# Performance work log

Measured on AMD Instinct MI355X. Metric: run time of the kernel, lower is better.

The kernel has to match this reference:

```python
import jax, jax.numpy as jnp
import numpy as np

TEMPERATURE = 0.1
EPS = 1e-12  # matches torch F.normalize eps


def _l2_normalize(x, axis=-1):
    n = jnp.sqrt(jnp.sum(x * x, axis=axis, keepdims=True))
    return x / jnp.maximum(n, EPS)


def setup_inputs() -> dict:
    key = jax.random.key(0)
    k1, k2, k3 = jax.random.split(key, 3)
    B, K, D, M = 128, 256, 256, 4
    local_vectors = jax.random.normal(k1, (B, K, D), dtype=jnp.float32)
    prototypes = jax.random.normal(k2, (K * M, D, 1, 1), dtype=jnp.float32)
    concepts_gt = jax.random.randint(k3, (B, K), 0, 2, dtype=jnp.int32)
    return {
        "local_vectors": local_vectors,
        "prototypes": prototypes,
        "concepts_gt": concepts_gt,
        "num_prototypes_per_concept": M,
    }


def reference(local_vectors, prototypes, concepts_gt, num_prototypes_per_concept):
    B, K, D = local_vectors.shape
    M = num_prototypes_per_concept
    protos = prototypes.reshape(K * M, D)  # squeeze(-1).squeeze(-1)
    ln = _l2_normalize(local_vectors)      # (B, K, D)
    pn = _l2_normalize(protos)             # (K*M, D)

    # similarities for every (b, k) query against all prototypes in one GEMM
    sims = jnp.einsum('bkd,pd->bkp', ln, pn) / TEMPERATURE  # (B, K, K*M)

    # logsumexp over all prototypes (shared across the M positives of a concept)
    lse = jax.nn.logsumexp(sims, axis=-1)  # (B, K)

    # sum of positive similarities: prototypes k*M..(k+1)*M-1 for concept k
    # diagonal over the two K axes, summed over m
    pos_sum = jnp.einsum('bkkm->bk', sims.reshape(B, K, K, M))  # (B, K)

    mask = (concepts_gt == 1).astype(sims.dtype)  # (B, K)
    Mf = jnp.asarray(M, sims.dtype)
    total = jnp.sum(mask * (Mf * lse - pos_sum))
    count = Mf * jnp.sum(mask)
    return jnp.where(count > 0, total / jnp.maximum(count, 1.0), jnp.zeros((), sims.dtype))
```

## Files before the change

### kernel.cpp

```cpp
#include <hip/hip_runtime.h>
#include <hip/hip_bf16.h>
#include <stdint.h>

#define KC   256
#define DD   256
#define NPROT 1024
#define NQ   32768

#define OFF_NSEL 0
#define OFF_TOT  8
#define OFF_TICK 16
#define OFF_SEL  256
#define OFF_PN   131328
#define OFF_QN   655616
#define QSLAB    1048576
#define OFF_ACC  17432832
#define ACC_STRIDE 32768

#define LN2F    0.69314718055994531f
#define C10L2E  14.426950408889634f

typedef __bf16 bf16x8 __attribute__((ext_vector_type(8)));
typedef float  f32x16 __attribute__((ext_vector_type(16)));

static __device__ __forceinline__ unsigned short f2bf(float x) {
  __hip_bfloat16 h = __float2bfloat16(x);
  return __builtin_bit_cast(unsigned short, h);
}

__global__ __launch_bounds__(256) void prep_k(const float* __restrict__ protos,
                                              unsigned char* __restrict__ ws) {
  if (blockIdx.x == 0 && threadIdx.x == 0) {
    *(int*)(ws + OFF_NSEL)  = 0;
    *(float*)(ws + OFF_TOT) = 0.0f;
    *(int*)(ws + OFF_TICK)  = 0;
  }
  const int w = threadIdx.x >> 6, lane = threadIdx.x & 63;
  const int r = blockIdx.x * 4 + w;
  const float4 v = ((const float4*)protos)[r * 64 + lane];
  float ss = v.x*v.x + v.y*v.y + v.z*v.z + v.w*v.w;
#pragma unroll
  for (int m = 1; m < 64; m <<= 1) ss += __shfl_xor(ss, m, 64);
  const float sc = C10L2E / fmaxf(sqrtf(ss), 1e-12f);
  uint2 p;
  p.x = (unsigned)f2bf(v.x * sc) | ((unsigned)f2bf(v.y * sc) << 16);
  p.y = (unsigned)f2bf(v.z * sc) | ((unsigned)f2bf(v.w * sc) << 16);
  *(uint2*)(ws + OFF_PN + (lane >> 2) * 32768 + r * 32 + (lane & 3) * 8) = p;
}

__global__ __launch_bounds__(512) void cqn_k(const int* __restrict__ gt,
                                             const float* __restrict__ lv,
                                             unsigned char* __restrict__ ws) {
  __shared__ int wcnt[8], wpre[8];
  __shared__ int sbase, btot;
  __shared__ int list[512];

  const int tid  = threadIdx.x;
  const int wv   = tid >> 6, lane = tid & 63;
  const int idx  = blockIdx.x * 512 + tid;

  const int selme = (gt[idx] == 1);
  const unsigned long long bal = __ballot(selme);
  if (lane == 0) wcnt[wv] = __popcll(bal);
  __syncthreads();
  if (tid == 0) {
    int tot = 0;
#pragma unroll
    for (int u = 0; u < 8; ++u) { wpre[u] = tot; tot += wcnt[u]; }
    btot  = tot;
    sbase = atomicAdd((int*)(ws + OFF_NSEL), tot);
  }
  __syncthreads();

  const int rank = __popcll(bal & ((1ull << lane) - 1ull));
  if (selme) {
    const int loc = wpre[wv] + rank;
    list[loc] = idx;
    ((int*)(ws + OFF_SEL))[sbase + loc] = idx;
  }
  __syncthreads();

  const int grp = tid >> 4, sub = tid & 15;
  const int nr  = btot, sb = sbase;
  for (int r = grp; r < nr; r += 32) {
    const int qi   = list[r];
    const int slot = sb + r;
    float4 vv[4];
#pragma unroll
    for (int u = 0; u < 4; ++u) vv[u] = ((const float4*)lv)[qi * 64 + u * 16 + sub];
    float ss = 0.0f;
#pragma unroll
    for (int u = 0; u < 4; ++u)
      ss += vv[u].x*vv[u].x + vv[u].y*vv[u].y + vv[u].z*vv[u].z + vv[u].w*vv[u].w;
#pragma unroll
    for (int m = 1; m < 16; m <<= 1) ss += __shfl_xor(ss, m, 64);
    const float sc = 1.0f / fmaxf(sqrtf(ss), 1e-12f);
#pragma unroll
    for (int u = 0; u < 4; ++u) {
      uint2 p;
      p.x = (unsigned)f2bf(vv[u].x * sc) | ((unsigned)f2bf(vv[u].y * sc) << 16);
      p.y = (unsigned)f2bf(vv[u].z * sc) | ((unsigned)f2bf(vv[u].w * sc) << 16);
      *(uint2*)(ws + OFF_QN + (u * 4 + (sub >> 2)) * QSLAB + slot * 32 + (sub & 3) * 8) = p;
    }
  }
}

__global__ __launch_bounds__(256) void main_k(unsigned char* __restrict__ ws) {
  __shared__ __align__(16) unsigned char Aq[64 * 512];

  const int tid  = threadIdx.x;
  const int w    = tid >> 6;
  const int lane = tid & 63;
  const int hi   = lane >> 5;
  const int l31  = lane & 31;

  const int tile = (int)(blockIdx.x & 511);
  const int c    = (int)(blockIdx.x >> 9);

  const int n_sel = *(const int*)(ws + OFF_NSEL);
  const int base  = tile * 64;
  if (base >= n_sel) return;
  const int* sel = (const int*)(ws + OFF_SEL);

  int valid[2], kqr[2];
#pragma unroll
  for (int j = 0; j < 2; ++j) {
    const int slot = base + j * 32 + l31;
    valid[j] = slot < n_sel;
    const int q = valid[j] ? sel[slot] : sel[base];
    kqr[j] = q & (KC - 1);
  }

  const unsigned char* pn0 = ws + OFF_PN + (c * 256 + w * 64 + l31) * 32 + hi * 16;
  const unsigned char* pn1 = pn0 + 32 * 32;

  bf16x8 pa0[4], pa1[4];
#pragma unroll
  for (int p = 0; p < 4; ++p) {
    pa0[p] = *(const bf16x8*)(pn0 + p * 32768);
    pa1[p] = *(const bf16x8*)(pn1 + p * 32768);
  }

  const unsigned char* qn = ws + OFF_QN;
  const int last = n_sel - 1;
#pragma unroll
  for (int i = 0; i < 4; ++i) {
    const int unit = i * 256 + tid;
    const int s = unit >> 6, r = unit & 63;
    const int slot = min(base + r, last);
    const unsigned char* src = qn + s * QSLAB + slot * 32;
    const uint4 d0 = *(const uint4*)(src);
    const uint4 d1 = *(const uint4*)(src + 16);
    const int swz = ((r & 7) << 4) ^ (((r >> 3) & 3) << 7);
    *(uint4*)(Aq + r * 512 + ((s * 32) ^ swz))      = d0;
    *(uint4*)(Aq + r * 512 + ((s * 32 + 16) ^ swz)) = d1;
  }
  __syncthreads();

  f32x16 acc[2][2];
#pragma unroll
  for (int i = 0; i < 2; ++i)
#pragma unroll
    for (int j = 0; j < 2; ++j)
#pragma unroll
      for (int t = 0; t < 16; ++t) acc[i][j][t] = 0.0f;

  const int bswz = ((l31 & 7) << 4) ^ (((l31 >> 3) & 3) << 7);

#pragma unroll
  for (int k = 0; k < 16; ++k) {
    const bf16x8 a0 = pa0[k & 3];
    const bf16x8 a1 = pa1[k & 3];
    pa0[k & 3] = *(const bf16x8*)(pn0 + ((k + 4) & 15) * 32768);
    pa1[k & 3] = *(const bf16x8*)(pn1 + ((k + 4) & 15) * 32768);
    const int bc = (k * 32 + hi * 16) ^ bswz;
    const bf16x8 b0 = *(const bf16x8*)(Aq + l31 * 512 + bc);
    const bf16x8 b1 = *(const bf16x8*)(Aq + (32 + l31) * 512 + bc);
    acc[0][0] = __builtin_amdgcn_mfma_f32_32x32x16_bf16(a0, b0, acc[0][0], 0, 0, 0);
    acc[0][1] = __builtin_amdgcn_mfma_f32_32x32x16_bf16(a0, b1, acc[0][1], 0, 0, 0);
    acc[1][0] = __builtin_amdgcn_mfma_f32_32x32x16_bf16(a1, b0, acc[1][0], 0, 0, 0);
    acc[1][1] = __builtin_amdgcn_mfma_f32_32x32x16_bf16(a1, b1, acc[1][1], 0, 0, 0);
  }

  float l_acc[2] = {0.f, 0.f}, p_acc[2] = {0.f, 0.f};
#pragma unroll
  for (int i = 0; i < 2; ++i) {
    const int r4base = c * 64 + w * 16 + i * 8 + hi;
#pragma unroll
    for (int j = 0; j < 2; ++j) {
      float l4[4] = {0.f, 0.f, 0.f, 0.f};
      float p4[4] = {0.f, 0.f, 0.f, 0.f};
#pragma unroll
      for (int g = 0; g < 4; ++g) {
        const float pm = (r4base + 2 * g == kqr[j]) ? 1.0f : 0.0f;
#pragma unroll
        for (int t = 0; t < 4; ++t) {
          const float y = acc[i][j][g * 4 + t];
          l4[t] += __builtin_amdgcn_exp2f(y);
          p4[t] = fmaf(pm, y, p4[t]);
        }
      }
      l_acc[j] += (l4[0] + l4[1]) + (l4[2] + l4[3]);
      p_acc[j] += (p4[0] + p4[1]) + (p4[2] + p4[3]);
    }
  }

#pragma unroll
  for (int j = 0; j < 2; ++j) {
    l_acc[j] += __shfl_xor(l_acc[j], 32, 64);
    p_acc[j] += __shfl_xor(p_acc[j], 32, 64);
  }
  if (hi == 0) {
    float2* accb = (float2*)(ws + OFF_ACC) + (c * 4 + w) * ACC_STRIDE;
#pragma unroll
    for (int j = 0; j < 2; ++j) {
      if (valid[j]) {
        const int slot = base + j * 32 + l31;
        float2 v2; v2.x = l_acc[j]; v2.y = p_acc[j];
        accb[slot] = v2;
      }
    }
  }
}

__global__ __launch_bounds__(256) void finish_k(unsigned char* __restrict__ ws,
                                                float* __restrict__ out) {
  __shared__ float accs[4];
  const int n_sel = *(const int*)(ws + OFF_NSEL);
  const int i = blockIdx.x * 256 + threadIdx.x;
  float contrib = 0.0f;
  if (i < n_sel) {
    const float2* a = (const float2*)(ws + OFF_ACC);
    float L = 0.0f, P = 0.0f;
#pragma unroll
    for (int u = 0; u < 16; ++u) {
      const float2 v = a[u * ACC_STRIDE + i];
      L += v.x; P += v.y;
    }
    contrib = LN2F * (4.0f * __builtin_amdgcn_logf(L) - P);
  }
#pragma unroll
  for (int m = 1; m < 64; m <<= 1) contrib += __shfl_xor(contrib, m, 64);
  if ((threadIdx.x & 63) == 0) accs[threadIdx.x >> 6] = contrib;
  __syncthreads();
  if (threadIdx.x == 0) {
    atomicAdd((float*)(ws + OFF_TOT), (accs[0] + accs[1]) + (accs[2] + accs[3]));
    __threadfence();
    const int t = atomicAdd((int*)(ws + OFF_TICK), 1);
    if (t == 127) {
      const float total = atomicAdd((float*)(ws + OFF_TOT), 0.0f);
      out[0] = (n_sel > 0) ? total / (4.0f * (float)n_sel) : 0.0f;
    }
  }
}

extern "C" void kernel_launch(void* const* d_in, const int* in_sizes, int n_in,
                              void* d_out, int out_size, void* d_ws, size_t ws_size,
                              hipStream_t stream) {
  const float* lv     = (const float*)d_in[0];
  const float* protos = (const float*)d_in[1];
  const int*   gt     = (const int*)d_in[2];
  (void)in_sizes; (void)n_in; (void)out_size; (void)ws_size;
  unsigned char* ws = (unsigned char*)d_ws;

  prep_k<<<256, 256, 0, stream>>>(protos, ws);
  cqn_k<<<64, 512, 0, stream>>>(gt, lv, ws);
  main_k<<<2048, 256, 0, stream>>>(ws);
  finish_k<<<128, 256, 0, stream>>>(ws, (float*)d_out);
}
```

Measured before the change: 37.82 us.

## Merge prototype prep with query compaction and halve prototype tile per block

The prototype normalisation and the query selection/compaction kernels are merged into one launch, with a block-index split between the two jobs. The workspace counters are now zeroed by an async memset. The main GEMM kernel now covers 128 prototypes per block instead of 256, doubling the grid, cutting MFMA accumulators per wave in half, and doubling the partial sums the finish kernel reduces. The intent is to save a launch and raise occupancy and parallelism. In exchange, each query tile is staged into LDS twice as often and an extra memset operation is added.

New measurement: 40.10 us. 1.06x slower.

```diff
diff --git a/kernel.cpp b/kernel.cpp
--- a/kernel.cpp
+++ b/kernel.cpp
@@ -28,36 +28,34 @@
   return __builtin_bit_cast(unsigned short, h);
 }
 
-__global__ __launch_bounds__(256) void prep_k(const float* __restrict__ protos,
+__global__ __launch_bounds__(512) void prep_k(const int* __restrict__ gt,
+                                              const float* __restrict__ lv,
+                                              const float* __restrict__ protos,
                                               unsigned char* __restrict__ ws) {
-  if (blockIdx.x == 0 && threadIdx.x == 0) {
-    *(int*)(ws + OFF_NSEL)  = 0;
-    *(float*)(ws + OFF_TOT) = 0.0f;
-    *(int*)(ws + OFF_TICK)  = 0;
-  }
-  const int w = threadIdx.x >> 6, lane = threadIdx.x & 63;
-  const int r = blockIdx.x * 4 + w;
-  const float4 v = ((const float4*)protos)[r * 64 + lane];
-  float ss = v.x*v.x + v.y*v.y + v.z*v.z + v.w*v.w;
-#pragma unroll
-  for (int m = 1; m < 64; m <<= 1) ss += __shfl_xor(ss, m, 64);
-  const float sc = C10L2E / fmaxf(sqrtf(ss), 1e-12f);
-  uint2 p;
-  p.x = (unsigned)f2bf(v.x * sc) | ((unsigned)f2bf(v.y * sc) << 16);
-  p.y = (unsigned)f2bf(v.z * sc) | ((unsigned)f2bf(v.w * sc) << 16);
-  *(uint2*)(ws + OFF_PN + (lane >> 2) * 32768 + r * 32 + (lane & 3) * 8) = p;
-}
-
-__global__ __launch_bounds__(512) void cqn_k(const int* __restrict__ gt,
-                                             const float* __restrict__ lv,
-                                             unsigned char* __restrict__ ws) {
+  const int blk = blockIdx.x;
+  const int tid = threadIdx.x;
+
+  if (blk < 128) {
+    const int wv = tid >> 6, lane = tid & 63;
+    const int r = blk * 8 + wv;
+    const float4 v = ((const float4*)protos)[r * 64 + lane];
+    float ss = v.x*v.x + v.y*v.y + v.z*v.z + v.w*v.w;
+#pragma unroll
+    for (int m = 1; m < 64; m <<= 1) ss += __shfl_xor(ss, m, 64);
+    const float sc = C10L2E / fmaxf(sqrtf(ss), 1e-12f);
+    uint2 p;
+    p.x = (unsigned)f2bf(v.x * sc) | ((unsigned)f2bf(v.y * sc) << 16);
+    p.y = (unsigned)f2bf(v.z * sc) | ((unsigned)f2bf(v.w * sc) << 16);
+    *(uint2*)(ws + OFF_PN + (lane >> 2) * 32768 + r * 32 + (lane & 3) * 8) = p;
+    return;
+  }
+
   __shared__ int wcnt[8], wpre[8];
   __shared__ int sbase, btot;
   __shared__ int list[512];
 
-  const int tid  = threadIdx.x;
   const int wv   = tid >> 6, lane = tid & 63;
-  const int idx  = blockIdx.x * 512 + tid;
+  const int idx  = (blk - 128) * 512 + tid;
 
   const int selme = (gt[idx] == 1);
   const unsigned long long bal = __ballot(selme);
@@ -131,15 +129,11 @@
     kqr[j] = q & (KC - 1);
   }
 
-  const unsigned char* pn0 = ws + OFF_PN + (c * 256 + w * 64 + l31) * 32 + hi * 16;
-  const unsigned char* pn1 = pn0 + 32 * 32;
-
-  bf16x8 pa0[4], pa1[4];
-#pragma unroll
-  for (int p = 0; p < 4; ++p) {
-    pa0[p] = *(const bf16x8*)(pn0 + p * 32768);
-    pa1[p] = *(const bf16x8*)(pn1 + p * 32768);
-  }
+  const unsigned char* pn = ws + OFF_PN + (c * 128 + w * 32 + l31) * 32 + hi * 16;
+
+  bf16x8 pa[4];
+#pragma unroll
+  for (int p = 0; p < 4; ++p) pa[p] = *(const bf16x8*)(pn + p * 32768);
 
   const unsigned char* qn = ws + OFF_QN;
   const int last = n_sel - 1;
@@ -157,52 +151,41 @@
   }
   __syncthreads();
 
-  f32x16 acc[2][2];
-#pragma unroll
-  for (int i = 0; i < 2; ++i)
-#pragma unroll
-    for (int j = 0; j < 2; ++j)
-#pragma unroll
-      for (int t = 0; t < 16; ++t) acc[i][j][t] = 0.0f;
+  f32x16 acc0, acc1;
+#pragma unroll
+  for (int t = 0; t < 16; ++t) { acc0[t] = 0.0f; acc1[t] = 0.0f; }
 
   const int bswz = ((l31 & 7) << 4) ^ (((l31 >> 3) & 3) << 7);
 
 #pragma unroll
   for (int k = 0; k < 16; ++k) {
-    const bf16x8 a0 = pa0[k & 3];
-    const bf16x8 a1 = pa1[k & 3];
-    pa0[k & 3] = *(const bf16x8*)(pn0 + ((k + 4) & 15) * 32768);
-    pa1[k & 3] = *(const bf16x8*)(pn1 + ((k + 4) & 15) * 32768);
+    const bf16x8 a = pa[k & 3];
+    pa[k & 3] = *(const bf16x8*)(pn + ((k + 4) & 15) * 32768);
     const int bc = (k * 32 + hi * 16) ^ bswz;
     const bf16x8 b0 = *(const bf16x8*)(Aq + l31 * 512 + bc);
     const bf16x8 b1 = *(const bf16x8*)(Aq + (32 + l31) * 512 + bc);
-    acc[0][0] = __builtin_amdgcn_mfma_f32_32x32x16_bf16(a0, b0, acc[0][0], 0, 0, 0);
-    acc[0][1] = __builtin_amdgcn_mfma_f32_32x32x16_bf16(a0, b1, acc[0][1], 0, 0, 0);
-    acc[1][0] = __builtin_amdgcn_mfma_f32_32x32x16_bf16(a1, b0, acc[1][0], 0, 0, 0);
-    acc[1][1] = __builtin_amdgcn_mfma_f32_32x32x16_bf16(a1, b1, acc[1][1], 0, 0, 0);
+    acc0 = __builtin_amdgcn_mfma_f32_32x32x16_bf16(a, b0, acc0, 0, 0, 0);
+    acc1 = __builtin_amdgcn_mfma_f32_32x32x16_bf16(a, b1, acc1, 0, 0, 0);
   }
 
   float l_acc[2] = {0.f, 0.f}, p_acc[2] = {0.f, 0.f};
-#pragma unroll
-  for (int i = 0; i < 2; ++i) {
-    const int r4base = c * 64 + w * 16 + i * 8 + hi;
-#pragma unroll
-    for (int j = 0; j < 2; ++j) {
-      float l4[4] = {0.f, 0.f, 0.f, 0.f};
-      float p4[4] = {0.f, 0.f, 0.f, 0.f};
-#pragma unroll
-      for (int g = 0; g < 4; ++g) {
-        const float pm = (r4base + 2 * g == kqr[j]) ? 1.0f : 0.0f;
-#pragma unroll
-        for (int t = 0; t < 4; ++t) {
-          const float y = acc[i][j][g * 4 + t];
-          l4[t] += __builtin_amdgcn_exp2f(y);
-          p4[t] = fmaf(pm, y, p4[t]);
-        }
+  const int r4base = c * 32 + w * 8 + hi;
+#pragma unroll
+  for (int j = 0; j < 2; ++j) {
+    float l4[4] = {0.f, 0.f, 0.f, 0.f};
+    float p4[4] = {0.f, 0.f, 0.f, 0.f};
+#pragma unroll
+    for (int g = 0; g < 4; ++g) {
+      const float pm = (r4base + 2 * g == kqr[j]) ? 1.0f : 0.0f;
+#pragma unroll
+      for (int t = 0; t < 4; ++t) {
+        const float y = (j == 0) ? acc0[g * 4 + t] : acc1[g * 4 + t];
+        l4[t] += __builtin_amdgcn_exp2f(y);
+        p4[t] = fmaf(pm, y, p4[t]);
       }
-      l_acc[j] += (l4[0] + l4[1]) + (l4[2] + l4[3]);
-      p_acc[j] += (p4[0] + p4[1]) + (p4[2] + p4[3]);
-    }
+    }
+    l_acc[j] = (l4[0] + l4[1]) + (l4[2] + l4[3]);
+    p_acc[j] = (p4[0] + p4[1]) + (p4[2] + p4[3]);
   }
 
 #pragma unroll
@@ -233,7 +216,7 @@
     const float2* a = (const float2*)(ws + OFF_ACC);
     float L = 0.0f, P = 0.0f;
 #pragma unroll
-    for (int u = 0; u < 16; ++u) {
+    for (int u = 0; u < 32; ++u) {
       const float2 v = a[u * ACC_STRIDE + i];
       L += v.x; P += v.y;
     }
@@ -263,8 +246,8 @@
   (void)in_sizes; (void)n_in; (void)out_size; (void)ws_size;
   unsigned char* ws = (unsigned char*)d_ws;
 
-  prep_k<<<256, 256, 0, stream>>>(protos, ws);
-  cqn_k<<<64, 512, 0, stream>>>(gt, lv, ws);
-  main_k<<<2048, 256, 0, stream>>>(ws);
+  hipMemsetAsync(d_ws, 0, 256, stream);
+  prep_k<<<192, 512, 0, stream>>>(gt, lv, protos, ws);
+  main_k<<<4096, 256, 0, stream>>>(ws);
   finish_k<<<128, 256, 0, stream>>>(ws, (float*)d_out);
 }
```
